# Kernel optimization log

Measured on AMD Instinct MI355X. Metric: run time of the kernel, lower is better.

The kernel has to match this reference:

```python
import jax, jax.numpy as jnp
import numpy as np

N, BOND, PHYS = 784, 4, 2
BS = 16384
STD = 1e-08


def setup_inputs() -> dict:
    key = jax.random.key(0)
    k1, k2 = jax.random.split(key)
    data = jax.random.randint(k1, (BS, N), 0, 2).astype(jnp.float32)
    bias = jnp.eye(BOND, dtype=jnp.float32)[:, :, None].repeat(PHYS, axis=2)  # (BOND,BOND,PHYS)
    tensors = STD * jax.random.normal(k2, (N, BOND, BOND, PHYS), dtype=jnp.float32) + bias
    return {"data": data, "tensors": tensors}


def reference(data, tensors):
    # data: (bs, n) in {0,1}; tensors: (n, D, D, P)
    bs, n = data.shape
    emb = jnp.stack([data, 1.0 - data], axis=2)  # (bs, n, P)
    # per-site transfer matrices for every sample: (n, bs, D, D)
    mats = jnp.einsum('nlri,bni->nblr', tensors, emb)
    left0 = mats[0][:, 0, :]  # (bs, D)  -- row 0 of site-0 matrix
    lx0 = jax.nn.log_softmax(tensors[0, 0, 0])  # (P,)

    def step(left, xs):
        t, m = xs  # t: (D, D, P), m: (bs, D, D)
        logits = left @ t[:, 0, :]              # (bs, P)
        lx = jax.nn.log_softmax(logits, axis=1)  # (bs, P)
        new_left = jnp.einsum('bl,blr->br', left, m)
        return new_left, lx

    _, lxs = jax.lax.scan(step, left0, (tensors[1:], mats[1:]))  # (n-1, bs, P)
    logx = jnp.concatenate(
        [jnp.broadcast_to(lx0, (1, bs, PHYS)), lxs], axis=0)  # (n, bs, P)
    logx = jnp.transpose(logx, (1, 0, 2))  # (bs, n, P)
    log_prob = logx[..., 0] * data + logx[..., 1] * (1.0 - data)
    return log_prob.sum(-1)  # (bs,)
```

## Files before the change

### kernel.cpp

```cpp
#include <hip/hip_runtime.h>

#define NSITES 784
#define BS_TOT 16384
#define KSEG 16
#define GSEG 49
#define NQUAD 12

typedef unsigned long long u64;

#define STEP_REGV(bitset, c0,c1,c2,c3,c4,c5,c6,c7, L0,L1,L2,L3, AN,AL) do { \
  float p00 = fmaf(L0, c0.x, fmaf(L1, c2.x, fmaf(L2, c4.x, L3 * c6.x))); \
  float p01 = fmaf(L0, c0.y, fmaf(L1, c2.y, fmaf(L2, c4.y, L3 * c6.y))); \
  float p10 = fmaf(L0, c0.z, fmaf(L1, c2.z, fmaf(L2, c4.z, L3 * c6.z))); \
  float p11 = fmaf(L0, c0.w, fmaf(L1, c2.w, fmaf(L2, c4.w, L3 * c6.w))); \
  float p20 = fmaf(L0, c1.x, fmaf(L1, c3.x, fmaf(L2, c5.x, L3 * c7.x))); \
  float p21 = fmaf(L0, c1.y, fmaf(L1, c3.y, fmaf(L2, c5.y, L3 * c7.y))); \
  float p30 = fmaf(L0, c1.z, fmaf(L1, c3.z, fmaf(L2, c5.z, L3 * c7.z))); \
  float p31 = fmaf(L0, c1.w, fmaf(L1, c3.w, fmaf(L2, c5.w, L3 * c7.w))); \
  bool s_ = (bitset); \
  float mx_ = fmaxf(p00, p01); \
  float ch_ = s_ ? p00 : p01; \
  AN += (ch_ - mx_); \
  float ad_ = fabsf(p00 - p01); \
  AL += __builtin_amdgcn_logf(1.0f + __builtin_amdgcn_exp2f(-ad_ * 1.4426950408889634f)); \
  L0 = s_ ? p00 : p01; \
  L1 = s_ ? p10 : p11; \
  L2 = s_ ? p20 : p21; \
  L3 = s_ ? p30 : p31; \
} while (0)

#define STEP(sbit, TP) do {                                                          \
    const float* t_ = (TP);                                                          \
    float p00 = fmaf(left0, t_[0],  fmaf(left1, t_[8],  fmaf(left2, t_[16], left3 * t_[24]))); \
    float p01 = fmaf(left0, t_[1],  fmaf(left1, t_[9],  fmaf(left2, t_[17], left3 * t_[25]))); \
    float p10 = fmaf(left0, t_[2],  fmaf(left1, t_[10], fmaf(left2, t_[18], left3 * t_[26]))); \
    float p11 = fmaf(left0, t_[3],  fmaf(left1, t_[11], fmaf(left2, t_[19], left3 * t_[27]))); \
    float p20 = fmaf(left0, t_[4],  fmaf(left1, t_[12], fmaf(left2, t_[20], left3 * t_[28]))); \
    float p21 = fmaf(left0, t_[5],  fmaf(left1, t_[13], fmaf(left2, t_[21], left3 * t_[29]))); \
    float p30 = fmaf(left0, t_[6],  fmaf(left1, t_[14], fmaf(left2, t_[22], left3 * t_[30]))); \
    float p31 = fmaf(left0, t_[7],  fmaf(left1, t_[15], fmaf(left2, t_[23], left3 * t_[31]))); \
    bool s_ = (sbit);                                                                \
    float mx_ = fmaxf(p00, p01);                                                     \
    float ch_ = s_ ? p00 : p01;                                                      \
    acc_nat += (ch_ - mx_);                                                          \
    float ad_ = fabsf(p00 - p01);                                                    \
    acc_l2 += __builtin_amdgcn_logf(1.0f + __builtin_amdgcn_exp2f(-ad_ * 1.4426950408889634f)); \
    left0 = s_ ? p00 : p01;                                                          \
    left1 = s_ ? p10 : p11;                                                          \
    left2 = s_ ? p20 : p21;                                                          \
    left3 = s_ ? p30 : p31;                                                          \
} while (0)

#define MM_ROW(Q, Pr) do {                                                           \
    Q.x = fmaf(Pr.x, m0.x, fmaf(Pr.y, m1.x, fmaf(Pr.z, m2.x, Pr.w * m3.x)));         \
    Q.y = fmaf(Pr.x, m0.y, fmaf(Pr.y, m1.y, fmaf(Pr.z, m2.y, Pr.w * m3.y)));         \
    Q.z = fmaf(Pr.x, m0.z, fmaf(Pr.y, m1.z, fmaf(Pr.z, m2.z, Pr.w * m3.z)));         \
    Q.w = fmaf(Pr.x, m0.w, fmaf(Pr.y, m1.w, fmaf(Pr.z, m2.w, Pr.w * m3.w)));         \
} while (0)

#define MM4(P0,P1,P2,P3) do { float4 Q0,Q1,Q2,Q3; \
    MM_ROW(Q0,P0); MM_ROW(Q1,P1); MM_ROW(Q2,P2); MM_ROW(Q3,P3); \
    P0=Q0; P1=Q1; P2=Q2; P3=Q3; } while (0)

__global__ __launch_bounds__(256) void fused_pre_kernel(const float* __restrict__ tensors,
                                                        const float* __restrict__ data,
                                                        float* __restrict__ QQ,
                                                        u64* __restrict__ packed) {
    if (blockIdx.x < KSEG) {
        __shared__ float sPP[24][4][16];
        const int k = blockIdx.x;
        const int t = threadIdx.x;
        const int n0 = k * GSEG;

        if (t < 96) {
            const int j = t >> 2, c2 = t & 3;
            const float* t0 = tensors + (size_t)(n0 + 2 * j) * 32;
            const float* t1 = tensors + (size_t)(n0 + 2 * j + 1) * 32;
            const int p0 = (c2 & 1) ? 0 : 1;
            const int p1 = (c2 & 2) ? 0 : 1;
            float A[4][4], B[4][4];
            #pragma unroll
            for (int l = 0; l < 4; ++l)
                #pragma unroll
                for (int r = 0; r < 4; ++r) {
                    A[l][r] = t0[l * 8 + r * 2 + p0];
                    B[l][r] = t1[l * 8 + r * 2 + p1];
                }
            #pragma unroll
            for (int a = 0; a < 4; ++a)
                #pragma unroll
                for (int bb = 0; bb < 4; ++bb)
                    sPP[j][c2][a * 4 + bb] =
                        fmaf(A[a][0], B[0][bb], fmaf(A[a][1], B[1][bb],
                        fmaf(A[a][2], B[2][bb], A[a][3] * B[3][bb])));
        }
        __syncthreads();

        if (t < 192) {
            const int q = t >> 4, c = t & 15;
            const float* A = sPP[2 * q][c & 3];
            const float* B = sPP[2 * q + 1][(c >> 2) & 3];
            float* dst = QQ + ((size_t)(k * NQUAD + q) * 16 + c) * 16;
            #pragma unroll
            for (int a = 0; a < 4; ++a)
                #pragma unroll
                for (int bb = 0; bb < 4; ++bb)
                    dst[a * 4 + bb] =
                        fmaf(A[a * 4 + 0], B[0 * 4 + bb], fmaf(A[a * 4 + 1], B[1 * 4 + bb],
                        fmaf(A[a * 4 + 2], B[2 * 4 + bb], A[a * 4 + 3] * B[3 * 4 + bb])));
        }
    } else {
        int gid  = (blockIdx.x - KSEG) * 256 + threadIdx.x;
        int row  = gid >> 6;
        int lane = threadIdx.x & 63;
        const float* r = data + (size_t)row * NSITES;
        #pragma unroll
        for (int w = 0; w < 12; ++w) {
            u64 m = __ballot(r[w * 64 + lane] == 1.0f);
            if (lane == 0) packed[(size_t)w * BS_TOT + row] = m;
        }
        float v = (lane < 16) ? r[768 + lane] : 0.0f;
        u64 m = __ballot((lane < 16) && (v == 1.0f));
        if (lane == 0) packed[(size_t)12 * BS_TOT + row] = m;
    }
}

__device__ __forceinline__ u64 bit_window(const u64* __restrict__ packed, int n0, int b) {
    int a0 = n0 >> 6, s = n0 & 63;
    u64 w0 = packed[(size_t)a0 * BS_TOT + b];
    u64 w1 = packed[(size_t)(a0 + 1) * BS_TOT + b];
    return s ? ((w0 >> s) | (w1 << (64 - s))) : w0;
}

__global__ __launch_bounds__(256) void phase1q_kernel(const float* __restrict__ tensors,
                                                      const u64* __restrict__ packed,
                                                      const float* __restrict__ QQ,
                                                      float* __restrict__ Pbuf) {
    const int b = blockIdx.x * 256 + threadIdx.x;
    const int k = blockIdx.y;
    const int n0 = k * GSEG;

    __shared__ __align__(16) float lt[NQUAD * 16 * 20];
    {
        const float4* src = (const float4*)(QQ + (size_t)k * NQUAD * 16 * 16);
        float4* dst = (float4*)lt;
        for (int e = threadIdx.x; e < NQUAD * 16 * 4; e += 256) {
            int q = e >> 6, c = (e >> 2) & 15, j = e & 3;
            dst[q * 80 + c * 5 + j] = src[e];
        }
    }
    __syncthreads();

    u64 win = bit_window(packed, n0, b);
    const float4* ltf4 = (const float4*)lt;

    float4 P0, P1, P2, P3;
    {
        const int c0 = (int)(win & 15ull);
        const float4* mi = ltf4 + (c0 * 5);
        P0 = mi[0]; P1 = mi[1]; P2 = mi[2]; P3 = mi[3];
    }
    #pragma unroll
    for (int q = 1; q < NQUAD; ++q) {
        const int cq = (int)((win >> (4 * q)) & 15ull);
        const float4* mi = ltf4 + (q * 80 + cq * 5);
        float4 m0 = mi[0], m1 = mi[1], m2 = mi[2], m3 = mi[3];
        MM4(P0, P1, P2, P3);
    }
    {
        const float* t48 = tensors + (size_t)(n0 + 48) * 32;
        const bool s48 = ((win >> 48) & 1ull) != 0;
        float4 m0 = make_float4(s48 ? t48[0]  : t48[1],  s48 ? t48[2]  : t48[3],
                                s48 ? t48[4]  : t48[5],  s48 ? t48[6]  : t48[7]);
        float4 m1 = make_float4(s48 ? t48[8]  : t48[9],  s48 ? t48[10] : t48[11],
                                s48 ? t48[12] : t48[13], s48 ? t48[14] : t48[15]);
        float4 m2 = make_float4(s48 ? t48[16] : t48[17], s48 ? t48[18] : t48[19],
                                s48 ? t48[20] : t48[21], s48 ? t48[22] : t48[23]);
        float4 m3 = make_float4(s48 ? t48[24] : t48[25], s48 ? t48[26] : t48[27],
                                s48 ? t48[28] : t48[29], s48 ? t48[30] : t48[31]);
        MM4(P0, P1, P2, P3);
    }

    float4* pb = (float4*)(Pbuf + ((size_t)k * BS_TOT + b) * 16);
    pb[0] = P0; pb[1] = P1; pb[2] = P2; pb[3] = P3;
}

__global__ __launch_bounds__(256) void scan_kernel(const float* __restrict__ Pbuf,
                                                   float* __restrict__ prefix) {
    int b = blockIdx.x * 256 + threadIdx.x;
    float l0 = 1.0f, l1 = 0.0f, l2 = 0.0f, l3 = 0.0f;
    const float4* base = (const float4*)Pbuf + (size_t)b * 4;
    #pragma unroll
    for (int kc = 0; kc < 3; ++kc) {
        float4 R[5][4];
        #pragma unroll
        for (int j = 0; j < 5; ++j) {
            const float4* pb = base + (size_t)(kc * 5 + j) * BS_TOT * 4;
            R[j][0] = pb[0]; R[j][1] = pb[1]; R[j][2] = pb[2]; R[j][3] = pb[3];
        }
        #pragma unroll
        for (int j = 0; j < 5; ++j) {
            const int k = kc * 5 + j;
            prefix[((size_t)k * 4 + 0) * BS_TOT + b] = l0;
            prefix[((size_t)k * 4 + 1) * BS_TOT + b] = l1;
            prefix[((size_t)k * 4 + 2) * BS_TOT + b] = l2;
            prefix[((size_t)k * 4 + 3) * BS_TOT + b] = l3;
            float n0 = fmaf(l0, R[j][0].x, fmaf(l1, R[j][1].x, fmaf(l2, R[j][2].x, l3 * R[j][3].x)));
            float n1 = fmaf(l0, R[j][0].y, fmaf(l1, R[j][1].y, fmaf(l2, R[j][2].y, l3 * R[j][3].y)));
            float n2 = fmaf(l0, R[j][0].z, fmaf(l1, R[j][1].z, fmaf(l2, R[j][2].z, l3 * R[j][3].z)));
            float n3 = fmaf(l0, R[j][0].w, fmaf(l1, R[j][1].w, fmaf(l2, R[j][2].w, l3 * R[j][3].w)));
            l0 = n0; l1 = n1; l2 = n2; l3 = n3;
        }
    }
    prefix[((size_t)15 * 4 + 0) * BS_TOT + b] = l0;
    prefix[((size_t)15 * 4 + 1) * BS_TOT + b] = l1;
    prefix[((size_t)15 * 4 + 2) * BS_TOT + b] = l2;
    prefix[((size_t)15 * 4 + 3) * BS_TOT + b] = l3;
}

__global__ __launch_bounds__(256) void walk4_kernel(const float* __restrict__ tensors,
                                                    const u64* __restrict__ packed,
                                                    const float* __restrict__ prefix,
                                                    float* __restrict__ res) {
    const int k  = blockIdx.y;
    const int n0 = k * GSEG;

    __shared__ __align__(16) float lt[GSEG * 32];
    {
        const float4* src = (const float4*)(tensors + (size_t)n0 * 32);
        float4* dst = (float4*)lt;
        for (int e = threadIdx.x; e < GSEG * 8; e += 256) dst[e] = src[e];
    }
    __syncthreads();

    const int t  = threadIdx.x;
    const int bA = blockIdx.x * 1024 + t;
    const int bB = bA + 256;
    const int bC = bA + 512;
    const int bD = bA + 768;

    u64 winA = bit_window(packed, n0, bA);
    u64 winB = bit_window(packed, n0, bB);
    u64 winC = bit_window(packed, n0, bC);
    u64 winD = bit_window(packed, n0, bD);

    const size_t pk = (size_t)k * 4 * BS_TOT;
    float lA0 = prefix[pk + 0 * BS_TOT + bA], lA1 = prefix[pk + 1 * BS_TOT + bA];
    float lA2 = prefix[pk + 2 * BS_TOT + bA], lA3 = prefix[pk + 3 * BS_TOT + bA];
    float lB0 = prefix[pk + 0 * BS_TOT + bB], lB1 = prefix[pk + 1 * BS_TOT + bB];
    float lB2 = prefix[pk + 2 * BS_TOT + bB], lB3 = prefix[pk + 3 * BS_TOT + bB];
    float lC0 = prefix[pk + 0 * BS_TOT + bC], lC1 = prefix[pk + 1 * BS_TOT + bC];
    float lC2 = prefix[pk + 2 * BS_TOT + bC], lC3 = prefix[pk + 3 * BS_TOT + bC];
    float lD0 = prefix[pk + 0 * BS_TOT + bD], lD1 = prefix[pk + 1 * BS_TOT + bD];
    float lD2 = prefix[pk + 2 * BS_TOT + bD], lD3 = prefix[pk + 3 * BS_TOT + bD];
    float anA = 0.0f, alA = 0.0f, anB = 0.0f, alB = 0.0f;
    float anC = 0.0f, alC = 0.0f, anD = 0.0f, alD = 0.0f;

    const float4* ltf4 = (const float4*)lt;
    #pragma unroll 7
    for (int i = 0; i < GSEG; ++i) {
        float4 c0 = ltf4[i * 8 + 0], c1 = ltf4[i * 8 + 1];
        float4 c2 = ltf4[i * 8 + 2], c3 = ltf4[i * 8 + 3];
        float4 c4 = ltf4[i * 8 + 4], c5 = ltf4[i * 8 + 5];
        float4 c6 = ltf4[i * 8 + 6], c7 = ltf4[i * 8 + 7];
        STEP_REGV(((winA >> i) & 1ull) != 0, c0,c1,c2,c3,c4,c5,c6,c7, lA0,lA1,lA2,lA3, anA,alA);
        STEP_REGV(((winB >> i) & 1ull) != 0, c0,c1,c2,c3,c4,c5,c6,c7, lB0,lB1,lB2,lB3, anB,alB);
        STEP_REGV(((winC >> i) & 1ull) != 0, c0,c1,c2,c3,c4,c5,c6,c7, lC0,lC1,lC2,lC3, anC,alC);
        STEP_REGV(((winD >> i) & 1ull) != 0, c0,c1,c2,c3,c4,c5,c6,c7, lD0,lD1,lD2,lD3, anD,alD);
    }

    const float LN2 = 0.6931471805599453f;
    res[(size_t)k * BS_TOT + bA] = anA - LN2 * alA;
    res[(size_t)k * BS_TOT + bB] = anB - LN2 * alB;
    res[(size_t)k * BS_TOT + bC] = anC - LN2 * alC;
    res[(size_t)k * BS_TOT + bD] = anD - LN2 * alD;
}

__global__ __launch_bounds__(256) void reduce_kernel(const float* __restrict__ res,
                                                     float* __restrict__ out) {
    int b = blockIdx.x * 256 + threadIdx.x;
    float a = 0.0f;
    #pragma unroll
    for (int k = 0; k < KSEG; ++k) a += res[(size_t)k * BS_TOT + b];
    out[b] = a;
}

__global__ __launch_bounds__(64) void amps_chain_kernel(
    const float* __restrict__ data, const float* __restrict__ tensors,
    float* __restrict__ out)
{
    int b = blockIdx.x * blockDim.x + threadIdx.x;
    if (b >= BS_TOT) return;
    const float* row = data + (size_t)b * NSITES;
    float left0 = 1.0f, left1 = 0.0f, left2 = 0.0f, left3 = 0.0f;
    float acc_nat = 0.0f, acc_l2 = 0.0f;
    for (int n = 0; n < NSITES; ++n) {
        STEP(row[n] == 1.0f, tensors + (size_t)n * 32);
    }
    out[b] = acc_nat - 0.6931471805599453f * acc_l2;
}

extern "C" void kernel_launch(void* const* d_in, const int* in_sizes, int n_in,
                              void* d_out, int out_size, void* d_ws, size_t ws_size,
                              hipStream_t stream) {
    const float* data    = (const float*)d_in[0];
    const float* tensors = (const float*)d_in[1];
    float* out = (float*)d_out;

    const size_t packed_bytes = (size_t)13 * BS_TOT * 8;
    const size_t Pbuf_bytes   = (size_t)(KSEG - 1) * BS_TOT * 16 * 4;
    const size_t QQ_bytes     = (size_t)KSEG * NQUAD * 16 * 16 * 4;
    const size_t prefix_bytes = (size_t)KSEG * 4 * BS_TOT * 4;
    const size_t res_bytes    = (size_t)KSEG * BS_TOT * 4;
    const size_t need = packed_bytes + Pbuf_bytes + QQ_bytes + prefix_bytes + res_bytes;

    if (ws_size < need) {
        hipLaunchKernelGGL(amps_chain_kernel, dim3(BS_TOT / 64), dim3(64), 0, stream,
                           data, tensors, out);
        return;
    }

    char* wsb = (char*)d_ws;
    u64*   packed = (u64*)wsb;
    float* Pbuf   = (float*)(wsb + packed_bytes);
    float* QQ     = (float*)(wsb + packed_bytes + Pbuf_bytes);
    float* prefix = (float*)(wsb + packed_bytes + Pbuf_bytes + QQ_bytes);
    float* res    = (float*)(wsb + packed_bytes + Pbuf_bytes + QQ_bytes + prefix_bytes);

    hipLaunchKernelGGL(fused_pre_kernel, dim3(KSEG + (BS_TOT * 64) / 256), dim3(256), 0, stream,
                       tensors, data, QQ, packed);
    hipLaunchKernelGGL(phase1q_kernel,   dim3(BS_TOT / 256, KSEG - 1), dim3(256), 0, stream,
                       tensors, packed, QQ, Pbuf);
    hipLaunchKernelGGL(scan_kernel,      dim3(BS_TOT / 256), dim3(256), 0, stream,
                       Pbuf, prefix);
    hipLaunchKernelGGL(walk4_kernel,     dim3(BS_TOT / 1024, KSEG), dim3(256), 0, stream,
                       tensors, packed, prefix, res);
    hipLaunchKernelGGL(reduce_kernel,    dim3(BS_TOT / 256), dim3(256), 0, stream, res, out);
}
```

Baseline: 57.75 us.

## Use pair tables instead of quad tables and replace reduce kernel with atomics

The precompute kernel now stops at 2-site pair product matrices (4 choices per pair) and no longer builds 4-site quad tables with a shared-memory pass. The phase-1 segment product therefore does 23 4x4 matmuls per sample instead of 11, with a much smaller shared table to load. Separately, the reduce kernel and its result buffer are removed: the walk kernel atomically adds its segment contributions into the output, which is zeroed by a memset first. This trades more per-sample arithmetic in phase 1 and atomic contention for one fewer launch and less precompute and memory traffic.

Result: slower. 62.19 us (+7.7%).

```diff
diff --git a/kernel.cpp b/kernel.cpp
--- a/kernel.cpp
+++ b/kernel.cpp
@@ -4,7 +4,7 @@
 #define BS_TOT 16384
 #define KSEG 16
 #define GSEG 49
-#define NQUAD 12
+#define NPAIR 24
 
 typedef unsigned long long u64;
 
@@ -64,14 +64,12 @@
 
 __global__ __launch_bounds__(256) void fused_pre_kernel(const float* __restrict__ tensors,
                                                         const float* __restrict__ data,
-                                                        float* __restrict__ QQ,
+                                                        float* __restrict__ PP,
                                                         u64* __restrict__ packed) {
     if (blockIdx.x < KSEG) {
-        __shared__ float sPP[24][4][16];
         const int k = blockIdx.x;
         const int t = threadIdx.x;
         const int n0 = k * GSEG;
-
         if (t < 96) {
             const int j = t >> 2, c2 = t & 3;
             const float* t0 = tensors + (size_t)(n0 + 2 * j) * 32;
@@ -86,28 +84,14 @@
                     A[l][r] = t0[l * 8 + r * 2 + p0];
                     B[l][r] = t1[l * 8 + r * 2 + p1];
                 }
-            #pragma unroll
-            for (int a = 0; a < 4; ++a)
-                #pragma unroll
-                for (int bb = 0; bb < 4; ++bb)
-                    sPP[j][c2][a * 4 + bb] =
-                        fmaf(A[a][0], B[0][bb], fmaf(A[a][1], B[1][bb],
-                        fmaf(A[a][2], B[2][bb], A[a][3] * B[3][bb])));
-        }
-        __syncthreads();
-
-        if (t < 192) {
-            const int q = t >> 4, c = t & 15;
-            const float* A = sPP[2 * q][c & 3];
-            const float* B = sPP[2 * q + 1][(c >> 2) & 3];
-            float* dst = QQ + ((size_t)(k * NQUAD + q) * 16 + c) * 16;
+            float* dst = PP + ((size_t)(k * NPAIR + j) * 4 + c2) * 16;
             #pragma unroll
             for (int a = 0; a < 4; ++a)
                 #pragma unroll
                 for (int bb = 0; bb < 4; ++bb)
                     dst[a * 4 + bb] =
-                        fmaf(A[a * 4 + 0], B[0 * 4 + bb], fmaf(A[a * 4 + 1], B[1 * 4 + bb],
-                        fmaf(A[a * 4 + 2], B[2 * 4 + bb], A[a * 4 + 3] * B[3 * 4 + bb])));
+                        fmaf(A[a][0], B[0][bb], fmaf(A[a][1], B[1][bb],
+                        fmaf(A[a][2], B[2][bb], A[a][3] * B[3][bb])));
         }
     } else {
         int gid  = (blockIdx.x - KSEG) * 256 + threadIdx.x;
@@ -132,21 +116,21 @@
     return s ? ((w0 >> s) | (w1 << (64 - s))) : w0;
 }
 
-__global__ __launch_bounds__(256) void phase1q_kernel(const float* __restrict__ tensors,
+__global__ __launch_bounds__(256) void phase1p_kernel(const float* __restrict__ tensors,
                                                       const u64* __restrict__ packed,
-                                                      const float* __restrict__ QQ,
+                                                      const float* __restrict__ PP,
                                                       float* __restrict__ Pbuf) {
     const int b = blockIdx.x * 256 + threadIdx.x;
     const int k = blockIdx.y;
     const int n0 = k * GSEG;
 
-    __shared__ __align__(16) float lt[NQUAD * 16 * 20];
+    __shared__ __align__(16) float lt[NPAIR * 4 * 20];
     {
-        const float4* src = (const float4*)(QQ + (size_t)k * NQUAD * 16 * 16);
+        const float4* src = (const float4*)(PP + (size_t)k * NPAIR * 4 * 16);
         float4* dst = (float4*)lt;
-        for (int e = threadIdx.x; e < NQUAD * 16 * 4; e += 256) {
-            int q = e >> 6, c = (e >> 2) & 15, j = e & 3;
-            dst[q * 80 + c * 5 + j] = src[e];
+        for (int e = threadIdx.x; e < NPAIR * 4 * 4; e += 256) {
+            int j = e >> 4, c = (e >> 2) & 3, r = e & 3;
+            dst[(j * 4 + c) * 5 + r] = src[e];
         }
     }
     __syncthreads();
@@ -156,14 +140,14 @@
 
     float4 P0, P1, P2, P3;
     {
-        const int c0 = (int)(win & 15ull);
-        const float4* mi = ltf4 + (c0 * 5);
+        const int c0 = (int)(win & 3ull);
+        const float4* mi = ltf4 + c0 * 5;
         P0 = mi[0]; P1 = mi[1]; P2 = mi[2]; P3 = mi[3];
     }
     #pragma unroll
-    for (int q = 1; q < NQUAD; ++q) {
-        const int cq = (int)((win >> (4 * q)) & 15ull);
-        const float4* mi = ltf4 + (q * 80 + cq * 5);
+    for (int j = 1; j < NPAIR; ++j) {
+        const int cj = (int)((win >> (2 * j)) & 3ull);
+        const float4* mi = ltf4 + (j * 4 + cj) * 5;
         float4 m0 = mi[0], m1 = mi[1], m2 = mi[2], m3 = mi[3];
         MM4(P0, P1, P2, P3);
     }
@@ -221,7 +205,7 @@
 __global__ __launch_bounds__(256) void walk4_kernel(const float* __restrict__ tensors,
                                                     const u64* __restrict__ packed,
                                                     const float* __restrict__ prefix,
-                                                    float* __restrict__ res) {
+                                                    float* __restrict__ out) {
     const int k  = blockIdx.y;
     const int n0 = k * GSEG;
 
@@ -270,19 +254,10 @@
     }
 
     const float LN2 = 0.6931471805599453f;
-    res[(size_t)k * BS_TOT + bA] = anA - LN2 * alA;
-    res[(size_t)k * BS_TOT + bB] = anB - LN2 * alB;
-    res[(size_t)k * BS_TOT + bC] = anC - LN2 * alC;
-    res[(size_t)k * BS_TOT + bD] = anD - LN2 * alD;
-}
-
-__global__ __launch_bounds__(256) void reduce_kernel(const float* __restrict__ res,
-                                                     float* __restrict__ out) {
-    int b = blockIdx.x * 256 + threadIdx.x;
-    float a = 0.0f;
-    #pragma unroll
-    for (int k = 0; k < KSEG; ++k) a += res[(size_t)k * BS_TOT + b];
-    out[b] = a;
+    atomicAdd(&out[bA], anA - LN2 * alA);
+    atomicAdd(&out[bB], anB - LN2 * alB);
+    atomicAdd(&out[bC], anC - LN2 * alC);
+    atomicAdd(&out[bD], anD - LN2 * alD);
 }
 
 __global__ __launch_bounds__(64) void amps_chain_kernel(
@@ -309,10 +284,9 @@
 
     const size_t packed_bytes = (size_t)13 * BS_TOT * 8;
     const size_t Pbuf_bytes   = (size_t)(KSEG - 1) * BS_TOT * 16 * 4;
-    const size_t QQ_bytes     = (size_t)KSEG * NQUAD * 16 * 16 * 4;
+    const size_t PP_bytes     = (size_t)KSEG * NPAIR * 4 * 16 * 4;
     const size_t prefix_bytes = (size_t)KSEG * 4 * BS_TOT * 4;
-    const size_t res_bytes    = (size_t)KSEG * BS_TOT * 4;
-    const size_t need = packed_bytes + Pbuf_bytes + QQ_bytes + prefix_bytes + res_bytes;
+    const size_t need = packed_bytes + Pbuf_bytes + PP_bytes + prefix_bytes;
 
     if (ws_size < need) {
         hipLaunchKernelGGL(amps_chain_kernel, dim3(BS_TOT / 64), dim3(64), 0, stream,
@@ -323,17 +297,17 @@
     char* wsb = (char*)d_ws;
     u64*   packed = (u64*)wsb;
     float* Pbuf   = (float*)(wsb + packed_bytes);
-    float* QQ     = (float*)(wsb + packed_bytes + Pbuf_bytes);
-    float* prefix = (float*)(wsb + packed_bytes + Pbuf_bytes + QQ_bytes);
-    float* res    = (float*)(wsb + packed_bytes + Pbuf_bytes + QQ_bytes + prefix_bytes);
+    float* PP     = (float*)(wsb + packed_bytes + Pbuf_bytes);
+    float* prefix = (float*)(wsb + packed_bytes + Pbuf_bytes + PP_bytes);
+
+    hipMemsetAsync(out, 0, (size_t)BS_TOT * 4, stream);
 
     hipLaunchKernelGGL(fused_pre_kernel, dim3(KSEG + (BS_TOT * 64) / 256), dim3(256), 0, stream,
-                       tensors, data, QQ, packed);
-    hipLaunchKernelGGL(phase1q_kernel,   dim3(BS_TOT / 256, KSEG - 1), dim3(256), 0, stream,
-                       tensors, packed, QQ, Pbuf);
+                       tensors, data, PP, packed);
+    hipLaunchKernelGGL(phase1p_kernel,   dim3(BS_TOT / 256, KSEG - 1), dim3(256), 0, stream,
+                       tensors, packed, PP, Pbuf);
     hipLaunchKernelGGL(scan_kernel,      dim3(BS_TOT / 256), dim3(256), 0, stream,
                        Pbuf, prefix);
     hipLaunchKernelGGL(walk4_kernel,     dim3(BS_TOT / 1024, KSEG), dim3(256), 0, stream,
-                       tensors, packed, prefix, res);
-    hipLaunchKernelGGL(reduce_kernel,    dim3(BS_TOT / 256), dim3(256), 0, stream, res, out);
-}
+                       tensors, packed, prefix, out);
+}
```

## Fuse reduction into walk kernel via atomics and software-pipeline LDS loads

Applied to the files above, without the earlier changes.

Drops the separate reduce kernel and its per-segment result buffer. The walk kernel now atomically adds each segment's log-probability into the output, which the preprocessing kernel zeroes first. The walk loop is rewritten to double-buffer the shared-memory tensor loads, so the next site's coefficients are fetched while the current site is computed, and its launch bounds are set to one block per CU. This saves a kernel launch and a global round trip, at the cost of 16-way float atomics per output element and a nondeterministic summation order.

Result: no change. 58.50 us (+1.3%).

```diff
diff --git a/kernel.cpp b/kernel.cpp
--- a/kernel.cpp
+++ b/kernel.cpp
@@ -65,12 +65,15 @@
 __global__ __launch_bounds__(256) void fused_pre_kernel(const float* __restrict__ tensors,
                                                         const float* __restrict__ data,
                                                         float* __restrict__ QQ,
-                                                        u64* __restrict__ packed) {
+                                                        u64* __restrict__ packed,
+                                                        float* __restrict__ out) {
     if (blockIdx.x < KSEG) {
         __shared__ float sPP[24][4][16];
         const int k = blockIdx.x;
         const int t = threadIdx.x;
         const int n0 = k * GSEG;
+
+        ((float4*)out)[k * 256 + t] = make_float4(0.f, 0.f, 0.f, 0.f);
 
         if (t < 96) {
             const int j = t >> 2, c2 = t & 3;
@@ -218,10 +221,21 @@
     prefix[((size_t)15 * 4 + 3) * BS_TOT + b] = l3;
 }
 
-__global__ __launch_bounds__(256) void walk4_kernel(const float* __restrict__ tensors,
-                                                    const u64* __restrict__ packed,
-                                                    const float* __restrict__ prefix,
-                                                    float* __restrict__ res) {
+#define LD8(r0,r1,r2,r3,r4,r5,r6,r7, base) do { \
+    r0 = (base)[0]; r1 = (base)[1]; r2 = (base)[2]; r3 = (base)[3]; \
+    r4 = (base)[4]; r5 = (base)[5]; r6 = (base)[6]; r7 = (base)[7]; } while (0)
+
+#define STEP4(bitpos, c0,c1,c2,c3,c4,c5,c6,c7) do { \
+    STEP_REGV(((winA >> (bitpos)) & 1ull) != 0, c0,c1,c2,c3,c4,c5,c6,c7, lA0,lA1,lA2,lA3, anA,alA); \
+    STEP_REGV(((winB >> (bitpos)) & 1ull) != 0, c0,c1,c2,c3,c4,c5,c6,c7, lB0,lB1,lB2,lB3, anB,alB); \
+    STEP_REGV(((winC >> (bitpos)) & 1ull) != 0, c0,c1,c2,c3,c4,c5,c6,c7, lC0,lC1,lC2,lC3, anC,alC); \
+    STEP_REGV(((winD >> (bitpos)) & 1ull) != 0, c0,c1,c2,c3,c4,c5,c6,c7, lD0,lD1,lD2,lD3, anD,alD); \
+} while (0)
+
+__global__ __launch_bounds__(256, 1) void walk4_kernel(const float* __restrict__ tensors,
+                                                       const u64* __restrict__ packed,
+                                                       const float* __restrict__ prefix,
+                                                       float* __restrict__ out) {
     const int k  = blockIdx.y;
     const int n0 = k * GSEG;
 
@@ -257,32 +271,24 @@
     float anC = 0.0f, alC = 0.0f, anD = 0.0f, alD = 0.0f;
 
     const float4* ltf4 = (const float4*)lt;
-    #pragma unroll 7
-    for (int i = 0; i < GSEG; ++i) {
-        float4 c0 = ltf4[i * 8 + 0], c1 = ltf4[i * 8 + 1];
-        float4 c2 = ltf4[i * 8 + 2], c3 = ltf4[i * 8 + 3];
-        float4 c4 = ltf4[i * 8 + 4], c5 = ltf4[i * 8 + 5];
-        float4 c6 = ltf4[i * 8 + 6], c7 = ltf4[i * 8 + 7];
-        STEP_REGV(((winA >> i) & 1ull) != 0, c0,c1,c2,c3,c4,c5,c6,c7, lA0,lA1,lA2,lA3, anA,alA);
-        STEP_REGV(((winB >> i) & 1ull) != 0, c0,c1,c2,c3,c4,c5,c6,c7, lB0,lB1,lB2,lB3, anB,alB);
-        STEP_REGV(((winC >> i) & 1ull) != 0, c0,c1,c2,c3,c4,c5,c6,c7, lC0,lC1,lC2,lC3, anC,alC);
-        STEP_REGV(((winD >> i) & 1ull) != 0, c0,c1,c2,c3,c4,c5,c6,c7, lD0,lD1,lD2,lD3, anD,alD);
-    }
+    float4 a0,a1,a2,a3,a4,a5,a6,a7;
+    LD8(a0,a1,a2,a3,a4,a5,a6,a7, ltf4);
+    #pragma unroll 1
+    for (int i = 0; i < GSEG - 1; i += 2) {
+        float4 b0,b1,b2,b3,b4,b5,b6,b7;
+        LD8(b0,b1,b2,b3,b4,b5,b6,b7, ltf4 + (i + 1) * 8);
+        STEP4(i, a0,a1,a2,a3,a4,a5,a6,a7);
+        const int i2 = (i + 2 < GSEG) ? (i + 2) : (GSEG - 1);
+        LD8(a0,a1,a2,a3,a4,a5,a6,a7, ltf4 + i2 * 8);
+        STEP4(i + 1, b0,b1,b2,b3,b4,b5,b6,b7);
+    }
+    STEP4(GSEG - 1, a0,a1,a2,a3,a4,a5,a6,a7);
 
     const float LN2 = 0.6931471805599453f;
-    res[(size_t)k * BS_TOT + bA] = anA - LN2 * alA;
-    res[(size_t)k * BS_TOT + bB] = anB - LN2 * alB;
-    res[(size_t)k * BS_TOT + bC] = anC - LN2 * alC;
-    res[(size_t)k * BS_TOT + bD] = anD - LN2 * alD;
-}
-
-__global__ __launch_bounds__(256) void reduce_kernel(const float* __restrict__ res,
-                                                     float* __restrict__ out) {
-    int b = blockIdx.x * 256 + threadIdx.x;
-    float a = 0.0f;
-    #pragma unroll
-    for (int k = 0; k < KSEG; ++k) a += res[(size_t)k * BS_TOT + b];
-    out[b] = a;
+    atomicAdd(&out[bA], anA - LN2 * alA);
+    atomicAdd(&out[bB], anB - LN2 * alB);
+    atomicAdd(&out[bC], anC - LN2 * alC);
+    atomicAdd(&out[bD], anD - LN2 * alD);
 }
 
 __global__ __launch_bounds__(64) void amps_chain_kernel(
@@ -311,8 +317,7 @@
     const size_t Pbuf_bytes   = (size_t)(KSEG - 1) * BS_TOT * 16 * 4;
     const size_t QQ_bytes     = (size_t)KSEG * NQUAD * 16 * 16 * 4;
     const size_t prefix_bytes = (size_t)KSEG * 4 * BS_TOT * 4;
-    const size_t res_bytes    = (size_t)KSEG * BS_TOT * 4;
-    const size_t need = packed_bytes + Pbuf_bytes + QQ_bytes + prefix_bytes + res_bytes;
+    const size_t need = packed_bytes + Pbuf_bytes + QQ_bytes + prefix_bytes;
 
     if (ws_size < need) {
         hipLaunchKernelGGL(amps_chain_kernel, dim3(BS_TOT / 64), dim3(64), 0, stream,
@@ -325,15 +330,13 @@
     float* Pbuf   = (float*)(wsb + packed_bytes);
     float* QQ     = (float*)(wsb + packed_bytes + Pbuf_bytes);
     float* prefix = (float*)(wsb + packed_bytes + Pbuf_bytes + QQ_bytes);
-    float* res    = (float*)(wsb + packed_bytes + Pbuf_bytes + QQ_bytes + prefix_bytes);
 
     hipLaunchKernelGGL(fused_pre_kernel, dim3(KSEG + (BS_TOT * 64) / 256), dim3(256), 0, stream,
-                       tensors, data, QQ, packed);
+                       tensors, data, QQ, packed, out);
     hipLaunchKernelGGL(phase1q_kernel,   dim3(BS_TOT / 256, KSEG - 1), dim3(256), 0, stream,
                        tensors, packed, QQ, Pbuf);
     hipLaunchKernelGGL(scan_kernel,      dim3(BS_TOT / 256), dim3(256), 0, stream,
                        Pbuf, prefix);
     hipLaunchKernelGGL(walk4_kernel,     dim3(BS_TOT / 1024, KSEG), dim3(256), 0, stream,
-                       tensors, packed, prefix, res);
-    hipLaunchKernelGGL(reduce_kernel,    dim3(BS_TOT / 256), dim3(256), 0, stream, res, out);
-}
+                       tensors, packed, prefix, out);
+}
```
